# Kernel optimization log

Measured on AMD Instinct MI355X. Metric: run time of the kernel, lower is better.

## Reference

```python
import jax, jax.numpy as jnp
import numpy as np
import math

D = 512; H = 8; NL = 6; VOCAB = 256; NC = 10; L = 1024; B = 4
DK = D // H
SCALE = math.sqrt(DK)
EMB_SCALE = math.sqrt(D)
EPS = 1e-5


def _pos_encoding(seq_len, d_model):
    pos = jnp.arange(seq_len, dtype=jnp.float32)[:, None]
    div = jnp.exp(-jnp.arange(0, d_model, 2, dtype=jnp.float32) / d_model * math.log(10000.0))
    pe = jnp.zeros((seq_len, d_model), dtype=jnp.float32)
    pe = pe.at[:, 0::2].set(jnp.sin(pos * div))
    pe = pe.at[:, 1::2].set(jnp.cos(pos * div))
    return pe


def _layer_norm(x, g, b):
    m = jnp.mean(x, axis=-1, keepdims=True)
    v = jnp.mean(jnp.square(x - m), axis=-1, keepdims=True)
    return (x - m) * jax.lax.rsqrt(v + EPS) * g + b


def setup_inputs() -> dict:
    key = jax.random.key(0)
    ks = jax.random.split(key, 18)
    s = 0.02  # keep activations in a sane range so softmax is not saturated
    return {
        "tokens": jax.random.randint(ks[0], (B, L), 0, VOCAB, dtype=jnp.int32),
        "emb_table": jax.random.normal(ks[1], (VOCAB, D), jnp.float32) * s,
        "Wq": jax.random.normal(ks[2], (NL, D, D), jnp.float32) * s,
        "bq": jax.random.normal(ks[3], (NL, D), jnp.float32) * s,
        "Wkv": jax.random.normal(ks[4], (NL, 2 * D, D), jnp.float32) * s,
        "bkv": jax.random.normal(ks[5], (NL, 2 * D), jnp.float32) * s,
        "Wo": jax.random.normal(ks[6], (NL, D, D), jnp.float32) * s,
        "bo": jax.random.normal(ks[7], (NL, D), jnp.float32) * s,
        "ln1_g": jnp.ones((NL, D), jnp.float32),
        "ln1_b": jnp.zeros((NL, D), jnp.float32),
        "W1": jax.random.normal(ks[8], (NL, 4 * D, D), jnp.float32) * s,
        "b1": jax.random.normal(ks[9], (NL, 4 * D), jnp.float32) * s,
        "W2": jax.random.normal(ks[10], (NL, D, 4 * D), jnp.float32) * s,
        "b2": jax.random.normal(ks[11], (NL, D), jnp.float32) * s,
        "ln2_g": jnp.ones((NL, D), jnp.float32),
        "ln2_b": jnp.zeros((NL, D), jnp.float32),
        "Wc": jax.random.normal(ks[12], (NC, D), jnp.float32) * s,
        "bc": jax.random.normal(ks[13], (NC,), jnp.float32) * s,
    }


def reference(tokens, emb_table, Wq, bq, Wkv, bkv, Wo, bo, ln1_g, ln1_b,
              W1, b1, W2, b2, ln2_g, ln2_b, Wc, bc):
    seq_len = tokens.shape[1]
    pe = _pos_encoding(seq_len, D)  # [L, D]
    x = emb_table[tokens] * EMB_SCALE + pe[None]  # [B, L, D]  (dropout = identity in eval)

    def block(x, p):
        wq, bq_, wkv, bkv_, wo, bo_, g1, be1, w1, bb1, w2, bb2, g2, be2 = p
        h = _layer_norm(x, g1, be1)
        q = h @ wq.T + bq_                       # [B, L, D]
        kv = h @ wkv.T + bkv_                    # [B, L, 2D]
        k, v = kv[..., :D], kv[..., D:]
        # split heads: [B, H, L, dk]
        q = q.reshape(*q.shape[:2], H, DK).transpose(0, 2, 1, 3)
        k = k.reshape(*k.shape[:2], H, DK).transpose(0, 2, 1, 3)
        v = v.reshape(*v.shape[:2], H, DK).transpose(0, 2, 1, 3)
        score = jnp.einsum('bhqd,bhkd->bhqk', q, k) / SCALE  # [B, H, L, L]
        attn = jax.nn.softmax(score, axis=-1)
        av = jnp.einsum('bhqk,bhkd->bhqd', attn, v)
        av = av.transpose(0, 2, 1, 3).reshape(*x.shape)      # merge heads
        x = x + (av @ wo.T + bo_)
        h2 = _layer_norm(x, g2, be2)
        ffn = jax.nn.relu(h2 @ w1.T + bb1) @ w2.T + bb2
        x = x + ffn
        return x, None

    params = (Wq, bq, Wkv, bkv, Wo, bo, ln1_g, ln1_b, W1, b1, W2, b2, ln2_g, ln2_b)
    x, _ = jax.lax.scan(block, x, params)
    return x @ Wc.T + bc  # [B, L, NC]
```

## Files before the change

kernel.cpp:

```cpp
#include <hip/hip_runtime.h>
#include <math.h>

#define D 512
#define HEADS 8
#define NLAYER 6
#define LSEQ 1024
#define BATCH 4
#define DKH 64
#define MTOK (BATCH*LSEQ)
#define EPS 1e-5f
#define EMB_SCALE 22.627416997969522f
#define INV_SCALE 0.125f

typedef __attribute__((ext_vector_type(8))) __bf16 bf16x8;
typedef __attribute__((ext_vector_type(4))) float f32x4;

__device__ __forceinline__ unsigned short f2bf(float x) {
    union { float f; unsigned u; } v; v.f = x;
    unsigned r = (v.u + 0x7FFFu + ((v.u >> 16) & 1u)) >> 16;
    return (unsigned short)r;
}
__device__ __forceinline__ unsigned pack2(float a, float b) {
    return (unsigned)f2bf(a) | ((unsigned)f2bf(b) << 16);
}
__device__ __forceinline__ void gl_lds16(const unsigned short* g, unsigned short* l) {
    __builtin_amdgcn_global_load_lds(
        (const __attribute__((address_space(1))) unsigned*)g,
        (__attribute__((address_space(3))) unsigned*)l, 16, 0, 0);
}
__device__ __forceinline__ void gload16(bf16x8& d, const unsigned short* p) {
    asm volatile("global_load_dwordx4 %0, %1, off" : "=v"(d) : "v"(p));
}

__global__ __launch_bounds__(128) void embed_kernel(
    const int* __restrict__ tokens, const float* __restrict__ emb,
    float* __restrict__ x)
{
    int row = blockIdx.x;
    int pos = row & (LSEQ - 1);
    int tok = tokens[row];
    int c = threadIdx.x * 4;
    float4 e = *(const float4*)(emb + (size_t)tok * D + c);
    float o[4] = {e.x, e.y, e.z, e.w};
#pragma unroll
    for (int i = 0; i < 4; ++i) {
        int col = c + i;
        int ii = col & ~1;
        float dv = expf(-(float)ii * (9.210340371976184f / (float)D));
        float a = (float)pos * dv;
        float pe = (col & 1) ? cosf(a) : sinf(a);
        o[i] = o[i] * EMB_SCALE + pe;
    }
    float4 r; r.x = o[0]; r.y = o[1]; r.z = o[2]; r.w = o[3];
    *(float4*)(x + (size_t)row * D + c) = r;
}

__global__ __launch_bounds__(256) void ln_kernel(
    const float* __restrict__ x, const float* __restrict__ g,
    const float* __restrict__ b, unsigned short* __restrict__ h)
{
    int lane = threadIdx.x & 63;
    int row = blockIdx.x * 4 + (threadIdx.x >> 6);
    const float* xr = x + (size_t)row * D + lane * 8;
    float4 v0 = *(const float4*)(xr);
    float4 v1 = *(const float4*)(xr + 4);
    float s = v0.x + v0.y + v0.z + v0.w + v1.x + v1.y + v1.z + v1.w;
#pragma unroll
    for (int off = 32; off; off >>= 1) s += __shfl_xor(s, off, 64);
    float m = s * (1.0f / D);
    float d0 = v0.x - m, d1 = v0.y - m, d2 = v0.z - m, d3 = v0.w - m;
    float d4 = v1.x - m, d5 = v1.y - m, d6 = v1.z - m, d7 = v1.w - m;
    float ss = d0*d0 + d1*d1 + d2*d2 + d3*d3 + d4*d4 + d5*d5 + d6*d6 + d7*d7;
#pragma unroll
    for (int off = 32; off; off >>= 1) ss += __shfl_xor(ss, off, 64);
    float inv = rsqrtf(ss * (1.0f / D) + EPS);
    const float* gp = g + lane * 8;
    const float* bp = b + lane * 8;
    float4 g0 = *(const float4*)(gp), g1 = *(const float4*)(gp + 4);
    float4 b0 = *(const float4*)(bp), b1 = *(const float4*)(bp + 4);
    uint4 o;
    o.x = pack2(d0 * inv * g0.x + b0.x, d1 * inv * g0.y + b0.y);
    o.y = pack2(d2 * inv * g0.z + b0.z, d3 * inv * g0.w + b0.w);
    o.z = pack2(d4 * inv * g1.x + b1.x, d5 * inv * g1.y + b1.y);
    o.w = pack2(d6 * inv * g1.z + b1.z, d7 * inv * g1.w + b1.w);
    *(uint4*)(h + (size_t)row * D + lane * 8) = o;
}

__global__ __launch_bounds__(256) void wconv_kernel(
    const float* __restrict__ Wq, const float* __restrict__ Wkv,
    const float* __restrict__ Wo, const float* __restrict__ W1,
    const float* __restrict__ W2, const float* __restrict__ bq,
    const float* __restrict__ bkv, unsigned short* __restrict__ dst,
    float* __restrict__ bias_out)
{
    if (blockIdx.x == 1536) {
        for (int i = threadIdx.x; i < 1536; i += 256)
            bias_out[i] = (i < 512) ? bq[i] : bkv[i - 512];
        return;
    }
    int gid = blockIdx.x * 256 + threadIdx.x;
    int e = gid * 8;
    const float* src;
    if      (e < 262144)  src = Wq  + e;
    else if (e < 786432)  src = Wkv + (e - 262144);
    else if (e < 1048576) src = Wo  + (e - 786432);
    else if (e < 2097152) src = W1  + (e - 1048576);
    else                  src = W2  + (e - 2097152);
    float4 a = *(const float4*)src;
    float4 b = *(const float4*)(src + 4);
    uint4 o;
    o.x = pack2(a.x, a.y); o.y = pack2(a.z, a.w);
    o.z = pack2(b.x, b.y); o.w = pack2(b.z, b.w);
    *(uint4*)(dst + e) = o;
}

template<int OMODE, int BM>
__global__ __launch_bounds__(256) void gemm_bf16(
    const unsigned short* __restrict__ A, const unsigned short* __restrict__ W,
    const float* __restrict__ bias, const float* __restrict__ X,
    void* __restrict__ C, void* __restrict__ C2, void* __restrict__ C3,
    int M, int N, int K)
{
    constexpr int WM = BM / 64;
    constexpr int WN = 4 / WM;
    constexpr int NI = 8 / WN;
    __shared__ __align__(16) unsigned short As[2][BM * 64];
    __shared__ __align__(16) unsigned short Bs[2][128 * 64];
    const int tid = threadIdx.x;
    const int wave = tid >> 6, lane = tid & 63;
    const int quad = lane >> 4, l16 = lane & 15;
    const int wm = wave / WN, wn = wave % WN;
    const int bm = blockIdx.y * BM, bn = blockIdx.x * 128;

    const int rS  = tid >> 3;
    const int csw = (((tid & 7) ^ (rS & 7)) << 3);
    const unsigned short* Asrc = A + (size_t)(bm + rS) * K + csw;
    const unsigned short* Bsrc = W + (size_t)(bn + rS) * K + csw;

    f32x4 acc[4][NI];
#pragma unroll
    for (int mi = 0; mi < 4; ++mi)
#pragma unroll
        for (int ni = 0; ni < NI; ++ni) acc[mi][ni] = (f32x4){0.f, 0.f, 0.f, 0.f};

    const int nt = K >> 6;

#pragma unroll
    for (int i = 0; i < BM / 32; ++i)
        gl_lds16(Asrc + (size_t)(i * 32) * K, &As[0][i * 2048 + tid * 8]);
#pragma unroll
    for (int i = 0; i < 4; ++i)
        gl_lds16(Bsrc + (size_t)(i * 32) * K, &Bs[0][i * 2048 + tid * 8]);
    __syncthreads();

    for (int t = 0; t < nt; ++t) {
        const int cur = t & 1;
        if (t + 1 < nt) {
            const int k0 = (t + 1) << 6;
#pragma unroll
            for (int i = 0; i < BM / 32; ++i)
                gl_lds16(Asrc + (size_t)(i * 32) * K + k0, &As[cur ^ 1][i * 2048 + tid * 8]);
#pragma unroll
            for (int i = 0; i < 4; ++i)
                gl_lds16(Bsrc + (size_t)(i * 32) * K + k0, &Bs[cur ^ 1][i * 2048 + tid * 8]);
        }
#pragma unroll
        for (int kc = 0; kc < 2; ++kc) {
            const int gch = (kc << 2) | quad;
            bf16x8 af[4], bfr[NI];
#pragma unroll
            for (int mi = 0; mi < 4; ++mi) {
                const int ra = wm * 64 + mi * 16 + l16;
                af[mi] = *(const bf16x8*)&As[cur][ra * 64 + ((gch ^ (ra & 7)) << 3)];
            }
#pragma unroll
            for (int ni = 0; ni < NI; ++ni) {
                const int rb = wn * (128 / WN) + ni * 16 + l16;
                bfr[ni] = *(const bf16x8*)&Bs[cur][rb * 64 + ((gch ^ (rb & 7)) << 3)];
            }
#pragma unroll
            for (int mi = 0; mi < 4; ++mi)
#pragma unroll
                for (int ni = 0; ni < NI; ++ni)
                    acc[mi][ni] = __builtin_amdgcn_mfma_f32_16x16x32_bf16(
                        af[mi], bfr[ni], acc[mi][ni], 0, 0, 0);
        }
        __syncthreads();
    }

    const int er = bm + wm * 64;
    const int ec = bn + wn * (128 / WN);

    if (OMODE == 0) {
        float* Cf = (float*)C;
#pragma unroll
        for (int ni = 0; ni < NI; ++ni) {
            int c = ec + ni * 16 + l16;
            float bv = bias[c];
#pragma unroll
            for (int mi = 0; mi < 4; ++mi)
#pragma unroll
                for (int r = 0; r < 4; ++r) {
                    int m = er + mi * 16 + quad * 4 + r;
                    Cf[(size_t)m * N + c] = acc[mi][ni][r] + bv + X[(size_t)m * N + c];
                }
        }
    } else if (OMODE == 1) {
        unsigned short* Cb = (unsigned short*)C;
#pragma unroll
        for (int ni = 0; ni < NI; ++ni) {
            int c = ec + ni * 16 + l16;
            float bv = bias[c];
#pragma unroll
            for (int mi = 0; mi < 4; ++mi)
#pragma unroll
                for (int r = 0; r < 4; ++r) {
                    int m = er + mi * 16 + quad * 4 + r;
                    Cb[(size_t)m * N + c] = f2bf(fmaxf(acc[mi][ni][r] + bv, 0.f));
                }
        }
    } else {
        if (bn < 512) {
            unsigned short* Qp = (unsigned short*)C;
#pragma unroll
            for (int ni = 0; ni < NI; ++ni) {
                int c = ec + ni * 16 + l16;
                float bv = bias[c];
                int hh = c >> 6, dd = c & 63;
                size_t cbase = (size_t)(dd >> 5) * 512 + (size_t)((dd >> 3) & 3) * 128 + (dd & 7);
#pragma unroll
                for (int mi = 0; mi < 4; ++mi)
#pragma unroll
                    for (int r = 0; r < 4; ++r) {
                        int m = er + mi * 16 + quad * 4 + r;
                        int b = m >> 10, t = m & 1023;
                        Qp[(size_t)(b * 8 + hh) * 65536 + (size_t)(t >> 4) * 1024
                           + cbase + (size_t)(t & 15) * 8] =
                            f2bf((acc[mi][ni][r] + bv) * INV_SCALE);
                    }
            }
        } else if (bn < 1024) {
            unsigned short* Kp = (unsigned short*)C2;
#pragma unroll
            for (int ni = 0; ni < NI; ++ni) {
                int c = ec + ni * 16 + l16;
                float bv = bias[c];
                int c2 = c - 512;
                int hh = c2 >> 6, dd = c2 & 63;
                size_t cbase = (size_t)(dd >> 5) * 512 + (size_t)((dd >> 3) & 3) * 128 + (dd & 7);
#pragma unroll
                for (int mi = 0; mi < 4; ++mi)
#pragma unroll
                    for (int r = 0; r < 4; ++r) {
                        int m = er + mi * 16 + quad * 4 + r;
                        int b = m >> 10, t = m & 1023;
                        Kp[(size_t)(b * 8 + hh) * 65536 + (size_t)(t >> 4) * 1024
                           + cbase + (size_t)(t & 15) * 8] =
                            f2bf(acc[mi][ni][r] + bv);
                    }
            }
        } else {
            unsigned short* Vp = (unsigned short*)C3;
#pragma unroll
            for (int ni = 0; ni < NI; ++ni) {
                int c = ec + ni * 16 + l16;
                float bv = bias[c];
                int c2 = c - 1024;
                int hh = c2 >> 6, dd = c2 & 63;
                size_t dbase = (size_t)(dd >> 4) * 16384 + (size_t)(dd & 15) * 8;
#pragma unroll
                for (int mi = 0; mi < 4; ++mi) {
                    int t0 = er + mi * 16 + quad * 4;
                    int b = t0 >> 10, tt = t0 & 1023;
                    ushort4 o;
                    o.x = f2bf(acc[mi][ni][0] + bv);
                    o.y = f2bf(acc[mi][ni][1] + bv);
                    o.z = f2bf(acc[mi][ni][2] + bv);
                    o.w = f2bf(acc[mi][ni][3] + bv);
                    *(ushort4*)(Vp + (size_t)(b * 8 + hh) * 65536 + dbase
                                + (size_t)(tt >> 5) * 512
                                + (size_t)((tt >> 3) & 3) * 128 + (tt & 7)) = o;
                }
            }
        }
    }
}

__global__ __launch_bounds__(256, 1) void attn_mfma(
    const unsigned short* __restrict__ Qb, const unsigned short* __restrict__ Kb,
    const unsigned short* __restrict__ Vt, unsigned short* __restrict__ av)
{
    __shared__ float Ol[4][32][68];
    __shared__ float Ls[4][32];
    const int tid = threadIdx.x;
    const int wave = tid >> 6, lane = tid & 63;
    const int quad = lane >> 4, l16 = lane & 15;
    const int bh = blockIdx.x & 31;
    const int b = bh >> 3, h = bh & 7;
    const int q0 = (blockIdx.x >> 5) * 32;

    const unsigned short* qp = Qb + (size_t)bh * 65536 + (size_t)(q0 >> 4) * 1024 + lane * 8;
    const unsigned short* kbase = Kb + (size_t)bh * 65536 + lane * 8;
    const unsigned short* vbase = Vt + (size_t)bh * 65536 + lane * 8;

    const int sA  = ((((2 * quad) & 3) << 4) + l16) << 2;
    const int sB2 = ((((2 * quad + 1) & 3) << 4) + l16) << 2;

    f32x4 o[2][4];
#pragma unroll
    for (int qs = 0; qs < 2; ++qs)
#pragma unroll
        for (int nf = 0; nf < 4; ++nf) o[qs][nf] = (f32x4){0.f, 0.f, 0.f, 0.f};
    float lp[2] = {0.f, 0.f};

    const int j0 = wave * 256;

    bf16x8 qf[2][2];
    gload16(qf[0][0], qp);
    gload16(qf[0][1], qp + 512);
    gload16(qf[1][0], qp + 1024);
    gload16(qf[1][1], qp + 1536);

    bf16x8 kc[2][8], vf[2][8];
#pragma unroll
    for (int nf = 0; nf < 4; ++nf) {
        gload16(kc[0][2 * nf],     kbase + (size_t)j0 * 64 + nf * 1024);
        gload16(kc[0][2 * nf + 1], kbase + (size_t)j0 * 64 + nf * 1024 + 512);
        gload16(vf[0][2 * nf],     vbase + (size_t)j0 * 16 + nf * 16384);
        gload16(vf[0][2 * nf + 1], vbase + (size_t)j0 * 16 + nf * 16384 + 512);
    }

#pragma unroll
    for (int it = 0; it < 4; ++it) {
        const int cur = it & 1, nxt = cur ^ 1;
        if (it < 3) {
            const int jn = j0 + (it + 1) * 64;
#pragma unroll
            for (int nf = 0; nf < 4; ++nf) {
                gload16(kc[nxt][2 * nf],     kbase + (size_t)jn * 64 + nf * 1024);
                gload16(kc[nxt][2 * nf + 1], kbase + (size_t)jn * 64 + nf * 1024 + 512);
                gload16(vf[nxt][2 * nf],     vbase + (size_t)jn * 16 + nf * 16384);
                gload16(vf[nxt][2 * nf + 1], vbase + (size_t)jn * 16 + nf * 16384 + 512);
            }
        }
        if (it < 3) asm volatile("s_waitcnt vmcnt(16)" ::: "memory");
        else        asm volatile("s_waitcnt vmcnt(0)"  ::: "memory");
        __builtin_amdgcn_sched_barrier(0);
        unsigned pk01[2][4], pk23[2][4];
#pragma unroll
        for (int nf = 0; nf < 4; ++nf)
#pragma unroll
            for (int qs = 0; qs < 2; ++qs) {
                f32x4 z = {0.f, 0.f, 0.f, 0.f};
                z = __builtin_amdgcn_mfma_f32_16x16x32_bf16(kc[cur][2 * nf], qf[qs][0], z, 0, 0, 0);
                z = __builtin_amdgcn_mfma_f32_16x16x32_bf16(kc[cur][2 * nf + 1], qf[qs][1], z, 0, 0, 0);
                float p0 = __expf(z[0]);
                float p1 = __expf(z[1]);
                float p2 = __expf(z[2]);
                float p3 = __expf(z[3]);
                lp[qs] += (p0 + p1) + (p2 + p3);
                pk01[qs][nf] = pack2(p0, p1);
                pk23[qs][nf] = pack2(p2, p3);
            }
#pragma unroll
        for (int qs = 0; qs < 2; ++qs) {
            union PU { unsigned d[4]; bf16x8 v; } f0, f1;
            unsigned a0, a1;
            a0 = (unsigned)__builtin_amdgcn_ds_bpermute(sA,  (int)pk01[qs][0]);
            a1 = (unsigned)__builtin_amdgcn_ds_bpermute(sA,  (int)pk01[qs][1]);
            f0.d[0] = (quad < 2) ? a0 : a1;
            a0 = (unsigned)__builtin_amdgcn_ds_bpermute(sA,  (int)pk23[qs][0]);
            a1 = (unsigned)__builtin_amdgcn_ds_bpermute(sA,  (int)pk23[qs][1]);
            f0.d[1] = (quad < 2) ? a0 : a1;
            a0 = (unsigned)__builtin_amdgcn_ds_bpermute(sB2, (int)pk01[qs][0]);
            a1 = (unsigned)__builtin_amdgcn_ds_bpermute(sB2, (int)pk01[qs][1]);
            f0.d[2] = (quad < 2) ? a0 : a1;
            a0 = (unsigned)__builtin_amdgcn_ds_bpermute(sB2, (int)pk23[qs][0]);
            a1 = (unsigned)__builtin_amdgcn_ds_bpermute(sB2, (int)pk23[qs][1]);
            f0.d[3] = (quad < 2) ? a0 : a1;
            a0 = (unsigned)__builtin_amdgcn_ds_bpermute(sA,  (int)pk01[qs][2]);
            a1 = (unsigned)__builtin_amdgcn_ds_bpermute(sA,  (int)pk01[qs][3]);
            f1.d[0] = (quad < 2) ? a0 : a1;
            a0 = (unsigned)__builtin_amdgcn_ds_bpermute(sA,  (int)pk23[qs][2]);
            a1 = (unsigned)__builtin_amdgcn_ds_bpermute(sA,  (int)pk23[qs][3]);
            f1.d[1] = (quad < 2) ? a0 : a1;
            a0 = (unsigned)__builtin_amdgcn_ds_bpermute(sB2, (int)pk01[qs][2]);
            a1 = (unsigned)__builtin_amdgcn_ds_bpermute(sB2, (int)pk01[qs][3]);
            f1.d[2] = (quad < 2) ? a0 : a1;
            a0 = (unsigned)__builtin_amdgcn_ds_bpermute(sB2, (int)pk23[qs][2]);
            a1 = (unsigned)__builtin_amdgcn_ds_bpermute(sB2, (int)pk23[qs][3]);
            f1.d[3] = (quad < 2) ? a0 : a1;
#pragma unroll
            for (int nf = 0; nf < 4; ++nf) {
                o[qs][nf] = __builtin_amdgcn_mfma_f32_16x16x32_bf16(f0.v, vf[cur][2 * nf], o[qs][nf], 0, 0, 0);
                o[qs][nf] = __builtin_amdgcn_mfma_f32_16x16x32_bf16(f1.v, vf[cur][2 * nf + 1], o[qs][nf], 0, 0, 0);
            }
        }
    }
#pragma unroll
    for (int qs = 0; qs < 2; ++qs)
#pragma unroll
        for (int nf = 0; nf < 4; ++nf)
#pragma unroll
            for (int r = 0; r < 4; ++r)
                Ol[wave][qs * 16 + quad * 4 + r][nf * 16 + l16] = o[qs][nf][r];
#pragma unroll
    for (int qs = 0; qs < 2; ++qs) {
        float ts = lp[qs];
        ts += __shfl_xor(ts, 16, 64);
        ts += __shfl_xor(ts, 32, 64);
        if (quad == 0) Ls[wave][qs * 16 + l16] = ts;
    }
    __syncthreads();
#pragma unroll
    for (int half = 0; half < 2; ++half)
#pragma unroll
        for (int r = 0; r < 4; ++r) {
            int qq = half * 16 + quad * 4 + r;
            float denom = Ls[0][qq] + Ls[1][qq] + Ls[2][qq] + Ls[3][qq];
            float v = Ol[0][qq][wave * 16 + l16] + Ol[1][qq][wave * 16 + l16]
                    + Ol[2][qq][wave * 16 + l16] + Ol[3][qq][wave * 16 + l16];
            int q = q0 + qq;
            av[((size_t)(b * 1024 + q)) * D + h * 64 + wave * 16 + l16] =
                f2bf(v / denom);
        }
}

__global__ __launch_bounds__(256) void cls_kernel(
    const float* __restrict__ x, const float* __restrict__ Wc,
    const float* __restrict__ bc, float* __restrict__ out)
{
    int lane = threadIdx.x & 63;
    int row = blockIdx.x * 4 + (threadIdx.x >> 6);
    const float* xr = x + (size_t)row * D + lane * 8;
    float4 v0 = *(const float4*)xr;
    float4 v1 = *(const float4*)(xr + 4);
    float acc[10];
#pragma unroll
    for (int c = 0; c < 10; ++c) {
        const float* wr = Wc + c * D + lane * 8;
        float4 w0 = *(const float4*)wr;
        float4 w1 = *(const float4*)(wr + 4);
        acc[c] = v0.x*w0.x + v0.y*w0.y + v0.z*w0.z + v0.w*w0.w
               + v1.x*w1.x + v1.y*w1.y + v1.z*w1.z + v1.w*w1.w;
    }
#pragma unroll
    for (int c = 0; c < 10; ++c)
#pragma unroll
        for (int off = 32; off; off >>= 1) acc[c] += __shfl_xor(acc[c], off, 64);
    if (lane == 0) {
#pragma unroll
        for (int c = 0; c < 10; ++c) out[(size_t)row * 10 + c] = acc[c] + bc[c];
    }
}

extern "C" void kernel_launch(void* const* d_in, const int* in_sizes, int n_in,
                              void* d_out, int out_size, void* d_ws, size_t ws_size,
                              hipStream_t stream)
{
    const int*   tokens = (const int*)  d_in[0];
    const float* emb    = (const float*)d_in[1];
    const float* Wq     = (const float*)d_in[2];
    const float* bq     = (const float*)d_in[3];
    const float* Wkv    = (const float*)d_in[4];
    const float* bkv    = (const float*)d_in[5];
    const float* Wo     = (const float*)d_in[6];
    const float* bo     = (const float*)d_in[7];
    const float* ln1g   = (const float*)d_in[8];
    const float* ln1b   = (const float*)d_in[9];
    const float* W1     = (const float*)d_in[10];
    const float* b1     = (const float*)d_in[11];
    const float* W2     = (const float*)d_in[12];
    const float* b2     = (const float*)d_in[13];
    const float* ln2g   = (const float*)d_in[14];
    const float* ln2b   = (const float*)d_in[15];
    const float* Wc     = (const float*)d_in[16];
    const float* bc     = (const float*)d_in[17];
    float* out = (float*)d_out;

    float* x  = (float*)d_ws;
    unsigned short* hb  = (unsigned short*)(x + (size_t)MTOK * D);
    unsigned short* Qb  = hb  + (size_t)MTOK * D;
    unsigned short* Kb  = Qb  + (size_t)32 * 1024 * 64;
    unsigned short* Vt  = Kb  + (size_t)32 * 1024 * 64;
    unsigned short* avb = Vt  + (size_t)32 * 1024 * 64;
    unsigned short* f1b = Qb;
    unsigned short* wl  = avb + (size_t)32 * 1024 * 64;
    float* wbias = (float*)(wl + (size_t)3145728);

    const size_t oWo = 786432, oW1 = 1048576, oW2 = 2097152;

    embed_kernel<<<MTOK, 128, 0, stream>>>(tokens, emb, x);

    for (int l = 0; l < NLAYER; ++l) {
        wconv_kernel<<<1537, 256, 0, stream>>>(
            Wq  + (size_t)l * 262144,  Wkv + (size_t)l * 524288,
            Wo  + (size_t)l * 262144,  W1  + (size_t)l * 1048576,
            W2  + (size_t)l * 1048576, bq + (size_t)l * 512,
            bkv + (size_t)l * 1024, wl, wbias);
        ln_kernel<<<MTOK / 4, 256, 0, stream>>>(x, ln1g + l * D, ln1b + l * D, hb);
        gemm_bf16<2,128><<<dim3(12, 32), 256, 0, stream>>>(
            hb, wl, wbias, nullptr, Qb, Kb, Vt, MTOK, 1536, 512);
        attn_mfma<<<1024, 256, 0, stream>>>(Qb, Kb, Vt, avb);
        gemm_bf16<0,64><<<dim3(4, 64), 256, 0, stream>>>(
            avb, wl + oWo, bo + l * D, x, x, nullptr, nullptr, MTOK, D, D);
        ln_kernel<<<MTOK / 4, 256, 0, stream>>>(x, ln2g + l * D, ln2b + l * D, hb);
        gemm_bf16<1,128><<<dim3(16, 32), 256, 0, stream>>>(
            hb, wl + oW1, b1 + l * 4 * D, nullptr, f1b, nullptr, nullptr, MTOK, 4 * D, D);
        gemm_bf16<0,64><<<dim3(4, 64), 256, 0, stream>>>(
            f1b, wl + oW2, b2 + l * D, x, x, nullptr, nullptr, MTOK, D, 4 * D);
    }

    cls_kernel<<<MTOK / 4, 256, 0, stream>>>(x, Wc, bc, out);
}
```

Measured before the change: 810.8 us.

## Triple-buffer LDS staging for BM=64 GEMM with explicit vmcnt waits

For the BM=64 GEMM variant, global-to-LDS loads move from two buffers to three, prefetching two K-tiles ahead. Explicit s_waitcnt vmcnt counters and raw barriers replace __syncthreads, so one tile's loads can stay in flight while the current tile is computed. This is meant to hide global memory latency better, at the cost of more LDS per block, which may reduce occupancy. The hand-tuned wait counts also depend on exactly how many loads each STAGE issues.

```diff
diff --git a/kernel.cpp b/kernel.cpp
--- a/kernel.cpp
+++ b/kernel.cpp
@@ -124,8 +124,10 @@
     constexpr int WM = BM / 64;
     constexpr int WN = 4 / WM;
     constexpr int NI = 8 / WN;
-    __shared__ __align__(16) unsigned short As[2][BM * 64];
-    __shared__ __align__(16) unsigned short Bs[2][128 * 64];
+    constexpr int NBUF = (BM == 64) ? 3 : 2;
+    constexpr int LPTA = BM / 32;
+    __shared__ __align__(16) unsigned short As[NBUF][BM * 64];
+    __shared__ __align__(16) unsigned short Bs[NBUF][128 * 64];
     const int tid = threadIdx.x;
     const int wave = tid >> 6, lane = tid & 63;
     const int quad = lane >> 4, l16 = lane & 15;
@@ -145,25 +147,16 @@
 
     const int nt = K >> 6;
 
-#pragma unroll
-    for (int i = 0; i < BM / 32; ++i)
-        gl_lds16(Asrc + (size_t)(i * 32) * K, &As[0][i * 2048 + tid * 8]);
-#pragma unroll
-    for (int i = 0; i < 4; ++i)
-        gl_lds16(Bsrc + (size_t)(i * 32) * K, &Bs[0][i * 2048 + tid * 8]);
-    __syncthreads();
-
-    for (int t = 0; t < nt; ++t) {
-        const int cur = t & 1;
-        if (t + 1 < nt) {
-            const int k0 = (t + 1) << 6;
-#pragma unroll
-            for (int i = 0; i < BM / 32; ++i)
-                gl_lds16(Asrc + (size_t)(i * 32) * K + k0, &As[cur ^ 1][i * 2048 + tid * 8]);
-#pragma unroll
-            for (int i = 0; i < 4; ++i)
-                gl_lds16(Bsrc + (size_t)(i * 32) * K + k0, &Bs[cur ^ 1][i * 2048 + tid * 8]);
-        }
+    auto STAGE = [&](int t, int buf) {
+        const int k0 = t << 6;
+#pragma unroll
+        for (int i = 0; i < LPTA; ++i)
+            gl_lds16(Asrc + (size_t)(i * 32) * K + k0, &As[buf][i * 2048 + tid * 8]);
+#pragma unroll
+        for (int i = 0; i < 4; ++i)
+            gl_lds16(Bsrc + (size_t)(i * 32) * K + k0, &Bs[buf][i * 2048 + tid * 8]);
+    };
+    auto COMPUTE = [&](int buf) {
 #pragma unroll
         for (int kc = 0; kc < 2; ++kc) {
             const int gch = (kc << 2) | quad;
@@ -171,12 +164,12 @@
 #pragma unroll
             for (int mi = 0; mi < 4; ++mi) {
                 const int ra = wm * 64 + mi * 16 + l16;
-                af[mi] = *(const bf16x8*)&As[cur][ra * 64 + ((gch ^ (ra & 7)) << 3)];
+                af[mi] = *(const bf16x8*)&As[buf][ra * 64 + ((gch ^ (ra & 7)) << 3)];
             }
 #pragma unroll
             for (int ni = 0; ni < NI; ++ni) {
                 const int rb = wn * (128 / WN) + ni * 16 + l16;
-                bfr[ni] = *(const bf16x8*)&Bs[cur][rb * 64 + ((gch ^ (rb & 7)) << 3)];
+                bfr[ni] = *(const bf16x8*)&Bs[buf][rb * 64 + ((gch ^ (rb & 7)) << 3)];
             }
 #pragma unroll
             for (int mi = 0; mi < 4; ++mi)
@@ -185,7 +178,38 @@
                     acc[mi][ni] = __builtin_amdgcn_mfma_f32_16x16x32_bf16(
                         af[mi], bfr[ni], acc[mi][ni], 0, 0, 0);
         }
+    };
+
+    if constexpr (BM == 64) {
+        STAGE(0, 0);
+        STAGE(1, 1);
+        asm volatile("s_waitcnt vmcnt(6)" ::: "memory");
+        __builtin_amdgcn_s_barrier();
+        __builtin_amdgcn_sched_barrier(0);
+        int cb = 0;
+        for (int t = 0; t < nt; ++t) {
+            const int sb = (cb >= 1) ? cb - 1 : 2;
+            if (t + 2 < nt) STAGE(t + 2, sb);
+            COMPUTE(cb);
+            asm volatile("s_waitcnt lgkmcnt(0)" ::: "memory");
+            __builtin_amdgcn_s_barrier();
+            if (t + 1 < nt) {
+                if (t + 2 < nt) asm volatile("s_waitcnt vmcnt(6)" ::: "memory");
+                else            asm volatile("s_waitcnt vmcnt(0)" ::: "memory");
+                __builtin_amdgcn_s_barrier();
+                __builtin_amdgcn_sched_barrier(0);
+            }
+            cb = (cb < 2) ? cb + 1 : 0;
+        }
+    } else {
+        STAGE(0, 0);
         __syncthreads();
+        for (int t = 0; t < nt; ++t) {
+            const int cur = t & 1;
+            if (t + 1 < nt) STAGE(t + 1, cur ^ 1);
+            COMPUTE(cur);
+            __syncthreads();
+        }
     }
 
     const int er = bm + wm * 64;
```

New measurement: 818.5 us. Within noise of the previous version (+0.9%).
